# Kernel tuning notes

Hardware: AMD Instinct MI355X
Metric: run time of the kernel (lower is better)

The kernel has to match this reference:

```python
import jax, jax.numpy as jnp
import numpy as np

B, N, F, H, OUT = 64, 512, 128, 256, 6


def setup_inputs() -> dict:
    key = jax.random.key(0)
    ks = jax.random.split(key, 20)
    s = 0.02
    inp = {
        "x": jax.random.normal(ks[0], (B * N, F), dtype=jnp.float32),
        "edge_index": jax.random.randint(ks[1], (2, 16), 0, B * N),
        "edge_weight": jax.random.uniform(ks[2], (16,), dtype=jnp.float32),
        "batch": jnp.repeat(jnp.arange(B, dtype=jnp.int64), N),
        "sigma": jax.random.uniform(ks[3], (1,), dtype=jnp.float32),
        "Wg": s * jax.random.normal(ks[4], (F, F)), "bg": jnp.zeros((F,)),
        "Wrel0": s * jax.random.normal(ks[5], (F, H)), "Wroot0": s * jax.random.normal(ks[6], (F, H)), "brel0": jnp.zeros((H,)),
        "Wrel1": s * jax.random.normal(ks[7], (H, H)), "Wroot1": s * jax.random.normal(ks[8], (H, H)), "brel1": jnp.zeros((H,)),
        "Wrel2": s * jax.random.normal(ks[9], (H, H)), "Wroot2": s * jax.random.normal(ks[10], (H, H)), "brel2": jnp.zeros((H,)),
        "W1": s * jax.random.normal(ks[11], (H, H)), "b1": jnp.zeros((H,)),
        "Wout": s * jax.random.normal(ks[12], (H, OUT)), "bout": jnp.zeros((OUT,)),
    }
    return inp


def _forward(x, sigma, Wg, bg, Wrel0, Wroot0, brel0, Wrel1, Wroot1, brel1,
             Wrel2, Wroot2, brel2, W1, b1, Wout, bout):
    # gdmLinear
    h = x @ Wg + bg                      # [B*N, F]
    hw = h.reshape(B, N, -1)             # to_dense_batch (equal-size windows)
    # pairwise squared distances per window -> Gaussian kernel
    sq = jnp.sum(hw * hw, axis=-1)       # [B, N]
    dist = jnp.maximum(sq[:, :, None] + sq[:, None, :]
                       - 2.0 * jnp.einsum('bnf,bmf->bnm', hw, hw), 0.0)
    A = jnp.exp(-dist / (2.0 * sigma[0] ** 2))   # [B, N, N], all > 0
    A = A * (1.0 - jnp.eye(N, dtype=A.dtype))    # nonzero extraction drops self-loops

    def conv(h, Wrel, Wroot, brel):
        # GraphConv: out_i = W_rel @ sum_j A[j,i] * h_j + b_rel + W_root @ h_i
        agg = jnp.einsum('bji,bjf->bif', A, h)
        return agg @ Wrel + brel + h @ Wroot

    h = hw
    h = jax.nn.relu(conv(h, Wrel0, Wroot0, brel0))
    h = jax.nn.relu(conv(h, Wrel1, Wroot1, brel1))
    h = conv(h, Wrel2, Wroot2, brel2)
    g = jnp.mean(h, axis=1)              # global_mean_pool (equal-size graphs)
    g = jax.nn.relu(g @ W1 + b1)
    return g @ Wout + bout               # [B, OUT]


def reference(x, edge_index, edge_weight, batch, sigma, Wg, bg,
              Wrel0, Wroot0, brel0, Wrel1, Wroot1, brel1,
              Wrel2, Wroot2, brel2, W1, b1, Wout, bout):
    # edge_index / edge_weight / batch inputs are recomputed internally by GdmGNN
    return _forward(x, sigma, Wg, bg, Wrel0, Wroot0, brel0, Wrel1, Wroot1, brel1,
                    Wrel2, Wroot2, brel2, W1, b1, Wout, bout)
```

## Files before the change

### kernel.cpp

```cpp
#include <hip/hip_runtime.h>
#include <math.h>

#define Bsz 64
#define Nn 512
#define Ff 128
#define Hh 256
#define OUTD 6
#define MTOT (Bsz * Nn)

typedef __bf16 bf16x8 __attribute__((ext_vector_type(8)));
typedef float f32x4 __attribute__((ext_vector_type(4)));
typedef int int4v __attribute__((ext_vector_type(4)));
typedef unsigned short ushort4v __attribute__((ext_vector_type(4)));

__device__ __forceinline__ unsigned short f2bf(float f) {
    unsigned u = __float_as_uint(f);
    u += 0x7FFFu + ((u >> 16) & 1u);
    return (unsigned short)(u >> 16);
}
__device__ __forceinline__ float bf2f(unsigned short s) {
    return __uint_as_float(((unsigned)s) << 16);
}

#define SWZ(r) (((r) ^ ((r) >> 2)) & 3)

__device__ __forceinline__ void async_ld16(const unsigned short* g, unsigned short* l) {
    __builtin_amdgcn_global_load_lds(
        (const __attribute__((address_space(1))) void*)g,
        (__attribute__((address_space(3))) void*)l,
        16, 0, 0);
}

#define LDH 40
#define TSZ (128 * 32)

__global__ __launch_bounds__(512) void gemm_ah(
    const unsigned short* __restrict__ HT, const unsigned short* __restrict__ Arows,
    unsigned short* __restrict__ agg,
    int F, long strideHT, long strideA, long strideC, int mTiles)
{
    int id = blockIdx.x;
    int bz = id & 63;
    int t = id >> 6;
    int bx = t % mTiles;
    int by = t / mTiles;

    HT += (long)bz * strideHT;
    Arows += (long)bz * strideA;
    agg += (long)bz * strideC;

    __shared__ unsigned short As[2 * TSZ];
    __shared__ unsigned short Bs[2 * TSZ];

    int tid = threadIdx.x;
    int lane = tid & 63;
    int wave = tid >> 6;
    int quad = lane >> 4, l16 = lane & 15;
    int wm = (wave >> 1) * 32, wn = (wave & 1) * 64;
    int m0 = bx * 128, n0 = by * 128;

    int sr = lane >> 2, sc = lane & 3;

    f32x4 acc[2][4] = {};

    auto issue = [&](int g) {
        int kk = g << 5;
        unsigned short* Ad = As + (g & 1) * TSZ;
        unsigned short* Bd = Bs + (g & 1) * TSZ;
        int r = wave * 16 + sr;
        int c = sc ^ SWZ(r);
        async_ld16(HT + (long)(m0 + r) * Nn + kk + c * 8, Ad + (wave * 16) * 32);
        async_ld16(Arows + (long)(n0 + r) * Nn + kk + c * 8, Bd + (wave * 16) * 32);
    };

    issue(0);
    for (int g = 0; g < (Nn >> 5); ++g) {
        __syncthreads();
        if (g + 1 < (Nn >> 5)) issue(g + 1);
        const unsigned short* Ab = As + (g & 1) * TSZ;
        const unsigned short* Bb = Bs + (g & 1) * TSZ;
        bf16x8 af[2], bfr[4];
        #pragma unroll
        for (int i = 0; i < 2; ++i) {
            int r = wm + i * 16 + l16;
            af[i] = *(const bf16x8*)&Ab[r * 32 + (quad ^ SWZ(r)) * 8];
        }
        #pragma unroll
        for (int j = 0; j < 4; ++j) {
            int r = wn + j * 16 + l16;
            bfr[j] = *(const bf16x8*)&Bb[r * 32 + (quad ^ SWZ(r)) * 8];
        }
        #pragma unroll
        for (int i = 0; i < 2; ++i)
            #pragma unroll
            for (int j = 0; j < 4; ++j)
                acc[i][j] = __builtin_amdgcn_mfma_f32_16x16x32_bf16(
                    af[i], bfr[j], acc[i][j], 0, 0, 0);
    }

    #pragma unroll
    for (int i = 0; i < 2; ++i) {
        int f = m0 + wm + i * 16 + quad * 4;
        #pragma unroll
        for (int j = 0; j < 4; ++j) {
            int node = n0 + wn + j * 16 + l16;
            f32x4 v = acc[i][j];
            ushort4v p;
            p[0] = f2bf(v[0]); p[1] = f2bf(v[1]); p[2] = f2bf(v[2]); p[3] = f2bf(v[3]);
            *(ushort4v*)&agg[(long)node * F + f] = p;
        }
    }
}

__global__ __launch_bounds__(512) void dense_t(
    const unsigned short* __restrict__ A0, const unsigned short* __restrict__ B0T,
    const unsigned short* __restrict__ A1, const unsigned short* __restrict__ B1T,
    const float* __restrict__ bias,
    unsigned short* __restrict__ outB, unsigned short* __restrict__ outT,
    int K0, int K1, int relu)
{
    int m0 = blockIdx.x * 128;
    int n0 = blockIdx.y * 128;

    __shared__ unsigned short As[2 * TSZ];
    __shared__ unsigned short Bs[2 * TSZ];

    int tid = threadIdx.x;
    int lane = tid & 63;
    int wave = tid >> 6;
    int quad = lane >> 4, l16 = lane & 15;
    int wm = (wave >> 1) * 32, wn = (wave & 1) * 64;

    int sr = lane >> 2, sc = lane & 3;

    int T0 = K0 >> 5, T1 = K1 >> 5;
    int T = T0 + T1;

    f32x4 acc[2][4] = {};

    auto issue = [&](int g) {
        const unsigned short* Ag; const unsigned short* Bg; int Kg, kk;
        if (g < T0) { Ag = A0; Bg = B0T; Kg = K0; kk = g << 5; }
        else        { Ag = A1; Bg = B1T; Kg = K1; kk = (g - T0) << 5; }
        unsigned short* Ad = As + (g & 1) * TSZ;
        unsigned short* Bd = Bs + (g & 1) * TSZ;
        int r = wave * 16 + sr;
        int c = sc ^ SWZ(r);
        async_ld16(Ag + (long)(m0 + r) * Kg + kk + c * 8, Ad + (wave * 16) * 32);
        async_ld16(Bg + (long)(n0 + r) * Kg + kk + c * 8, Bd + (wave * 16) * 32);
    };

    issue(0);
    for (int g = 0; g < T; ++g) {
        __syncthreads();
        if (g + 1 < T) issue(g + 1);
        const unsigned short* Ab = As + (g & 1) * TSZ;
        const unsigned short* Bb = Bs + (g & 1) * TSZ;
        bf16x8 af[2], bfr[4];
        #pragma unroll
        for (int i = 0; i < 2; ++i) {
            int r = wm + i * 16 + l16;
            af[i] = *(const bf16x8*)&Ab[r * 32 + (quad ^ SWZ(r)) * 8];
        }
        #pragma unroll
        for (int j = 0; j < 4; ++j) {
            int r = wn + j * 16 + l16;
            bfr[j] = *(const bf16x8*)&Bb[r * 32 + (quad ^ SWZ(r)) * 8];
        }
        #pragma unroll
        for (int i = 0; i < 2; ++i)
            #pragma unroll
            for (int j = 0; j < 4; ++j)
                acc[i][j] = __builtin_amdgcn_mfma_f32_16x16x32_bf16(
                    af[i], bfr[j], acc[i][j], 0, 0, 0);
    }

    #pragma unroll
    for (int i = 0; i < 2; ++i) {
        int of = m0 + wm + i * 16 + quad * 4;
        float b0 = bias[of + 0], b1 = bias[of + 1];
        float b2 = bias[of + 2], b3 = bias[of + 3];
        #pragma unroll
        for (int j = 0; j < 4; ++j) {
            int node = n0 + wn + j * 16 + l16;
            f32x4 v = acc[i][j];
            float o0 = v[0] + b0, o1 = v[1] + b1, o2 = v[2] + b2, o3 = v[3] + b3;
            if (relu) {
                o0 = fmaxf(o0, 0.f); o1 = fmaxf(o1, 0.f);
                o2 = fmaxf(o2, 0.f); o3 = fmaxf(o3, 0.f);
            }
            ushort4v p;
            p[0] = f2bf(o0); p[1] = f2bf(o1); p[2] = f2bf(o2); p[3] = f2bf(o3);
            *(ushort4v*)&outB[(long)node * Hh + of] = p;
            if (outT) {
                long base = ((long)(node >> 9) * Hh) * 512 + (node & 511);
                outT[base + (long)(of + 0) * 512] = p[0];
                outT[base + (long)(of + 1) * 512] = p[1];
                outT[base + (long)(of + 2) * 512] = p[2];
                outT[base + (long)(of + 3) * 512] = p[3];
            }
        }
    }
}

__global__ __launch_bounds__(256) void prep_h0(
    const float* __restrict__ x, const float* __restrict__ Wg,
    const float* __restrict__ bg,
    const float* __restrict__ Wrel0, const float* __restrict__ Wroot0,
    const float* __restrict__ Wrel1, const float* __restrict__ Wroot1,
    unsigned short* __restrict__ T0, unsigned short* __restrict__ T1,
    unsigned short* __restrict__ T2, unsigned short* __restrict__ T3,
    unsigned short* __restrict__ WgT,
    float* __restrict__ w,
    unsigned short* __restrict__ h0b, unsigned short* __restrict__ h0T,
    float* __restrict__ sqv)
{
    if (blockIdx.x < 960) {
        int idx = blockIdx.x * 256 + threadIdx.x;
        if (idx >= 212992) { w[idx - 212992] = 0.f; return; }
        if (idx >= 196608) {
            int e = idx - 196608;
            int o = e >> 7, i = e & 127;
            WgT[e] = f2bf(Wg[(long)i * 128 + o]);
            return;
        }
        const float* src; unsigned short* dst; int kin; int e;
        if      (idx <  32768) { src = Wrel0;  dst = T0; kin = 128; e = idx; }
        else if (idx <  65536) { src = Wroot0; dst = T1; kin = 128; e = idx - 32768; }
        else if (idx < 131072) { src = Wrel1;  dst = T2; kin = 256; e = idx - 65536; }
        else                   { src = Wroot1; dst = T3; kin = 256; e = idx - 131072; }
        int o = (kin == 128) ? (e >> 7) : (e >> 8);
        int i = e & (kin - 1);
        dst[e] = f2bf(src[(long)i * 256 + o]);
        return;
    }

    __shared__ unsigned short As[128 * LDH];
    __shared__ unsigned short Bs[128 * LDH];
    __shared__ float rsq[128];

    int tid = threadIdx.x;
    int lane = tid & 63;
    int wave = tid >> 6;
    int quad = lane >> 4, l16 = lane & 15;
    int wm = (wave >> 1) * 64, wn = (wave & 1) * 64;
    int m0 = (blockIdx.x - 960) * 128;

    f32x4 acc[4][4] = {};

    for (int k0 = 0; k0 < Ff; k0 += 32) {
        __syncthreads();
        #pragma unroll
        for (int l = 0; l < 2; ++l) {
            int idx = tid + l * 256;
            int r = idx >> 2, ch = idx & 3;
            const float* px = x + (long)(m0 + r) * Ff + k0 + ch * 8;
            float4 xa = *(const float4*)px;
            float4 xb = *(const float4*)(px + 4);
            ushort4v pa, pb;
            pa[0] = f2bf(xa.x); pa[1] = f2bf(xa.y); pa[2] = f2bf(xa.z); pa[3] = f2bf(xa.w);
            pb[0] = f2bf(xb.x); pb[1] = f2bf(xb.y); pb[2] = f2bf(xb.z); pb[3] = f2bf(xb.w);
            *(ushort4v*)&As[r * LDH + ch * 8] = pa;
            *(ushort4v*)&As[r * LDH + ch * 8 + 4] = pb;
            int kk = k0 + ch * 8;
            ushort4v qa, qb;
            #pragma unroll
            for (int u = 0; u < 4; ++u) qa[u] = f2bf(Wg[(long)(kk + u) * 128 + r]);
            #pragma unroll
            for (int u = 0; u < 4; ++u) qb[u] = f2bf(Wg[(long)(kk + 4 + u) * 128 + r]);
            *(ushort4v*)&Bs[r * LDH + ch * 8] = qa;
            *(ushort4v*)&Bs[r * LDH + ch * 8 + 4] = qb;
        }
        __syncthreads();
        bf16x8 af[4], bfr[4];
        #pragma unroll
        for (int i = 0; i < 4; ++i)
            af[i] = *(const bf16x8*)&As[(wm + i * 16 + l16) * LDH + quad * 8];
        #pragma unroll
        for (int j = 0; j < 4; ++j)
            bfr[j] = *(const bf16x8*)&Bs[(wn + j * 16 + l16) * LDH + quad * 8];
        #pragma unroll
        for (int i = 0; i < 4; ++i)
            #pragma unroll
            for (int j = 0; j < 4; ++j)
                acc[i][j] = __builtin_amdgcn_mfma_f32_16x16x32_bf16(
                    af[i], bfr[j], acc[i][j], 0, 0, 0);
    }

    if (tid < 128) rsq[tid] = 0.f;
    __syncthreads();

    #pragma unroll
    for (int i = 0; i < 4; ++i) {
        int lrow = wm + i * 16 + quad * 4;
        int mb = m0 + lrow;
        float rp0 = 0.f, rp1 = 0.f, rp2 = 0.f, rp3 = 0.f;
        #pragma unroll
        for (int j = 0; j < 4; ++j) {
            int n = wn + j * 16 + l16;
            f32x4 v = acc[i][j];
            float bv = bg[n];
            unsigned short s0 = f2bf(v[0] + bv), s1 = f2bf(v[1] + bv);
            unsigned short s2 = f2bf(v[2] + bv), s3 = f2bf(v[3] + bv);
            h0b[(long)(mb + 0) * Ff + n] = s0;
            h0b[(long)(mb + 1) * Ff + n] = s1;
            h0b[(long)(mb + 2) * Ff + n] = s2;
            h0b[(long)(mb + 3) * Ff + n] = s3;
            ushort4v p; p[0] = s0; p[1] = s1; p[2] = s2; p[3] = s3;
            long ti = ((long)(mb >> 9) * Ff + n) * 512 + (mb & 511);
            *(ushort4v*)&h0T[ti] = p;
            float f0 = bf2f(s0), f1 = bf2f(s1), f2 = bf2f(s2), f3 = bf2f(s3);
            rp0 += f0 * f0; rp1 += f1 * f1; rp2 += f2 * f2; rp3 += f3 * f3;
        }
        #pragma unroll
        for (int m = 1; m < 16; m <<= 1) {
            rp0 += __shfl_xor(rp0, m);
            rp1 += __shfl_xor(rp1, m);
            rp2 += __shfl_xor(rp2, m);
            rp3 += __shfl_xor(rp3, m);
        }
        if (l16 == 0) {
            atomicAdd(&rsq[lrow + 0], rp0);
            atomicAdd(&rsq[lrow + 1], rp1);
            atomicAdd(&rsq[lrow + 2], rp2);
            atomicAdd(&rsq[lrow + 3], rp3);
        }
    }
    __syncthreads();
    if (tid < 128) sqv[m0 + tid] = rsq[tid];
}

__global__ __launch_bounds__(512) void gram_A_mfma(
    const unsigned short* __restrict__ h0b, const float* __restrict__ sqv,
    const float* __restrict__ sigma, unsigned short* __restrict__ Aout,
    float* __restrict__ w)
{
    const int ti_[10] = {0,0,0,0,1,1,1,2,2,3};
    const int tj_[10] = {0,1,2,3,1,2,3,2,3,3};
    int id = blockIdx.x;
    int b = id & 63;
    int tt = id >> 6;
    int i0 = ti_[tt] * 128, j0 = tj_[tt] * 128;
    bool offdiag = (i0 != j0);

    const unsigned short* H = h0b + (long)b * Nn * Ff;
    const float* SQ = sqv + (long)b * Nn;
    unsigned short* Ab = Aout + (long)b * Nn * Nn;

    __shared__ unsigned short Is[2 * TSZ];
    __shared__ unsigned short Js[2 * TSZ];
    __shared__ float rsum[128];
    __shared__ float csum[128];

    int tid = threadIdx.x;
    int lane = tid & 63;
    int wave = tid >> 6;
    int quad = lane >> 4, l16 = lane & 15;
    int wm = (wave >> 1) * 32, wn = (wave & 1) * 64;

    int sr = lane >> 2, sc = lane & 3;

    f32x4 acc[2][4] = {};

    auto issue = [&](int g) {
        int kk = g << 5;
        unsigned short* Id = Is + (g & 1) * TSZ;
        unsigned short* Jd = Js + (g & 1) * TSZ;
        int r = wave * 16 + sr;
        int c = sc ^ SWZ(r);
        async_ld16(H + (long)(i0 + r) * Ff + kk + c * 8, Id + (wave * 16) * 32);
        async_ld16(H + (long)(j0 + r) * Ff + kk + c * 8, Jd + (wave * 16) * 32);
    };

    issue(0);
    for (int g = 0; g < (Ff >> 5); ++g) {
        __syncthreads();
        if (g + 1 < (Ff >> 5)) issue(g + 1);
        const unsigned short* Ib = Is + (g & 1) * TSZ;
        const unsigned short* Jb = Js + (g & 1) * TSZ;
        bf16x8 af[2], bfr[4];
        #pragma unroll
        for (int i = 0; i < 2; ++i) {
            int r = wm + i * 16 + l16;
            af[i] = *(const bf16x8*)&Ib[r * 32 + (quad ^ SWZ(r)) * 8];
        }
        #pragma unroll
        for (int j = 0; j < 4; ++j) {
            int r = wn + j * 16 + l16;
            bfr[j] = *(const bf16x8*)&Jb[r * 32 + (quad ^ SWZ(r)) * 8];
        }
        #pragma unroll
        for (int i = 0; i < 2; ++i)
            #pragma unroll
            for (int j = 0; j < 4; ++j)
                acc[i][j] = __builtin_amdgcn_mfma_f32_16x16x32_bf16(
                    af[i], bfr[j], acc[i][j], 0, 0, 0);
    }

    if (tid < 128) { rsum[tid] = 0.f; csum[tid] = 0.f; }
    __syncthreads();

    float s = sigma[0];
    float inv2s2 = 1.0f / (2.0f * s * s);
    float cj[4] = {0.f, 0.f, 0.f, 0.f};
    #pragma unroll
    for (int i = 0; i < 2; ++i) {
        int lrow = wm + i * 16 + quad * 4;
        int rb = i0 + lrow;
        float rs0 = 0.f, rs1 = 0.f, rs2 = 0.f, rs3 = 0.f;
        #pragma unroll
        for (int j = 0; j < 4; ++j) {
            int c = j0 + wn + j * 16 + l16;
            float sqc = SQ[c];
            f32x4 v = acc[i][j];
            ushort4v pk;
            float av[4];
            #pragma unroll
            for (int r4 = 0; r4 < 4; ++r4) {
                int r = rb + r4;
                float d = fmaxf(SQ[r] + sqc - 2.0f * v[r4], 0.0f);
                unsigned short a = (r == c) ? (unsigned short)0
                                            : f2bf(__expf(-d * inv2s2));
                pk[r4] = a;
                av[r4] = bf2f(a);
            }
            *(ushort4v*)&Ab[(long)c * Nn + rb] = pk;
            if (offdiag) {
                Ab[(long)(rb + 0) * Nn + c] = pk[0];
                Ab[(long)(rb + 1) * Nn + c] = pk[1];
                Ab[(long)(rb + 2) * Nn + c] = pk[2];
                Ab[(long)(rb + 3) * Nn + c] = pk[3];
                cj[j] += av[0] + av[1] + av[2] + av[3];
            }
            rs0 += av[0]; rs1 += av[1]; rs2 += av[2]; rs3 += av[3];
        }
        #pragma unroll
        for (int m = 1; m < 16; m <<= 1) {
            rs0 += __shfl_xor(rs0, m);
            rs1 += __shfl_xor(rs1, m);
            rs2 += __shfl_xor(rs2, m);
            rs3 += __shfl_xor(rs3, m);
        }
        if (l16 == 0) {
            atomicAdd(&rsum[lrow + 0], rs0);
            atomicAdd(&rsum[lrow + 1], rs1);
            atomicAdd(&rsum[lrow + 2], rs2);
            atomicAdd(&rsum[lrow + 3], rs3);
        }
    }
    if (offdiag) {
        #pragma unroll
        for (int j = 0; j < 4; ++j) {
            cj[j] += __shfl_xor(cj[j], 16);
            cj[j] += __shfl_xor(cj[j], 32);
        }
        if (quad == 0) {
            #pragma unroll
            for (int j = 0; j < 4; ++j)
                atomicAdd(&csum[wn + j * 16 + l16], cj[j]);
        }
    }
    __syncthreads();
    if (tid < 128) {
        atomicAdd(&w[(long)b * Nn + i0 + tid], rsum[tid]);
        if (offdiag) atomicAdd(&w[(long)b * Nn + j0 + tid], csum[tid]);
    }
}

__global__ __launch_bounds__(256) void reduce_h2(
    const unsigned short* __restrict__ h2b, const float* __restrict__ w,
    float* __restrict__ vpart, float* __restrict__ mpart)
{
    int b = blockIdx.x;
    int jc = blockIdx.y;
    int c = threadIdx.x;
    const unsigned short* H = h2b + ((long)b * Nn + jc * 64) * Hh + c;
    const float* wp = w + (long)b * Nn + jc * 64;
    float vp = 0.f, mp = 0.f;
    #pragma unroll 4
    for (int j = 0; j < 64; ++j) {
        float val = bf2f(H[(long)j * Hh]);
        mp += val;
        vp += wp[j] * val;
    }
    long o = ((long)b * 8 + jc) * Hh + c;
    vpart[o] = vp;
    mpart[o] = mp;
}

__global__ __launch_bounds__(256) void head_kernel(
    const float* __restrict__ vpart, const float* __restrict__ mpart,
    const float* __restrict__ Wrel2, const float* __restrict__ Wroot2,
    const float* __restrict__ brel2,
    const float* __restrict__ W1, const float* __restrict__ b1,
    const float* __restrict__ Wout, const float* __restrict__ bout,
    float* __restrict__ out)
{
    int b = blockIdx.x;
    int j = threadIdx.x;
    __shared__ float vs[Hh], ms[Hh], gs[Hh], g2[Hh];
    float vp = 0.f, mp = 0.f;
    #pragma unroll
    for (int p = 0; p < 8; ++p) {
        long o = ((long)b * 8 + p) * Hh + j;
        vp += vpart[o];
        mp += mpart[o];
    }
    vs[j] = vp * (1.0f / (float)Nn);
    ms[j] = mp * (1.0f / (float)Nn);
    __syncthreads();
    float s = brel2[j];
    for (int c = 0; c < Hh; ++c)
        s += vs[c] * Wrel2[c * Hh + j] + ms[c] * Wroot2[c * Hh + j];
    gs[j] = s;
    __syncthreads();
    float t = b1[j];
    for (int k = 0; k < Hh; ++k) t += gs[k] * W1[k * Hh + j];
    g2[j] = fmaxf(t, 0.f);
    __syncthreads();
    if (j < OUTD) {
        float s2 = bout[j];
        for (int k = 0; k < Hh; ++k) s2 += g2[k] * Wout[k * OUTD + j];
        out[b * OUTD + j] = s2;
    }
}

extern "C" void kernel_launch(void* const* d_in, const int* in_sizes, int n_in,
                              void* d_out, int out_size, void* d_ws, size_t ws_size,
                              hipStream_t stream) {
    const float* x      = (const float*)d_in[0];
    const float* sigma  = (const float*)d_in[4];
    const float* Wg     = (const float*)d_in[5];
    const float* bg     = (const float*)d_in[6];
    const float* Wrel0  = (const float*)d_in[7];
    const float* Wroot0 = (const float*)d_in[8];
    const float* brel0  = (const float*)d_in[9];
    const float* Wrel1  = (const float*)d_in[10];
    const float* Wroot1 = (const float*)d_in[11];
    const float* brel1  = (const float*)d_in[12];
    const float* Wrel2  = (const float*)d_in[13];
    const float* Wroot2 = (const float*)d_in[14];
    const float* brel2  = (const float*)d_in[15];
    const float* W1     = (const float*)d_in[16];
    const float* b1     = (const float*)d_in[17];
    const float* Wout   = (const float*)d_in[18];
    const float* bout   = (const float*)d_in[19];
    float* out = (float*)d_out;

    char* ws = (char*)d_ws;
    unsigned short* WgT  = (unsigned short*)(ws + 0);
    unsigned short* h0b  = (unsigned short*)(ws + 16777216);
    unsigned short* h0T  = (unsigned short*)(ws + 25165824);
    float*          sq   = (float*)(ws + 33554432);
    unsigned short* Aadj = (unsigned short*)(ws + 33685504);
    unsigned short* agg  = (unsigned short*)(ws + 67239936);
    unsigned short* h1b  = (unsigned short*)(ws + 84017152);
    unsigned short* h1T  = (unsigned short*)(ws + 100794368);
    unsigned short* h2b  = (unsigned short*)(ws + 117571584);
    unsigned short* WrelT0  = (unsigned short*)(ws + 167903232);
    unsigned short* WrootT0 = (unsigned short*)(ws + 167968768);
    unsigned short* WrelT1  = (unsigned short*)(ws + 168034304);
    unsigned short* WrootT1 = (unsigned short*)(ws + 168165376);
    float*          w     = (float*)(ws + 168558592);
    float*          vpart = (float*)(ws + 168689664);
    float*          mpart = (float*)(ws + 169213952);

    prep_h0<<<1216, 256, 0, stream>>>(x, Wg, bg, Wrel0, Wroot0, Wrel1, Wroot1,
                                      WrelT0, WrootT0, WrelT1, WrootT1, WgT,
                                      w, h0b, h0T, sq);

    gram_A_mfma<<<dim3(10 * Bsz, 1, 1), 512, 0, stream>>>(h0b, sq, sigma, Aadj, w);

    gemm_ah<<<dim3(4 * Bsz, 1, 1), 512, 0, stream>>>(
        h0T, Aadj, agg, Ff,
        (long)Ff * Nn, (long)Nn * Nn, (long)Nn * Ff, 1);
    dense_t<<<dim3(2, MTOT / 128), 512, 0, stream>>>(
        WrelT0, agg, WrootT0, h0b, brel0, h1b, h1T, Ff, Ff, 1);

    gemm_ah<<<dim3(8 * Bsz, 1, 1), 512, 0, stream>>>(
        h1T, Aadj, agg, Hh,
        (long)Hh * Nn, (long)Nn * Nn, (long)Nn * Hh, 2);
    dense_t<<<dim3(2, MTOT / 128), 512, 0, stream>>>(
        WrelT1, agg, WrootT1, h1b, brel1, h2b, nullptr, Hh, Hh, 1);

    reduce_h2<<<dim3(Bsz, 8), 256, 0, stream>>>(h2b, w, vpart, mpart);
    head_kernel<<<Bsz, 256, 0, stream>>>(vpart, mpart, Wrel2, Wroot2, brel2,
                                         W1, b1, Wout, bout, out);
}
```

Baseline: 235.8 us.

## Fuse final pooling into dense_t and compute full Gram tiles without symmetric mirroring

The weighted and plain per-graph column sums of h2 are now computed in the epilogue of the second dense_t via a template flag, so h2 is no longer written to memory and the separate reduce_h2 kernel is dropped. The Gram/adjacency kernel changes from 10 upper-triangular tiles with scattered transposed mirror writes to all 16 tiles per graph, each doing only coalesced writes and row sums. This trades about 60% more Gram MFMA and exp work for removing strided scalar stores, column-sum atomics and one kernel launch plus an h2 round trip.

Result: faster. 229.6 us (-2.6%).

```diff
diff --git a/kernel.cpp b/kernel.cpp
--- a/kernel.cpp
+++ b/kernel.cpp
@@ -112,11 +112,13 @@
     }
 }
 
+template<int POOL>
 __global__ __launch_bounds__(512) void dense_t(
     const unsigned short* __restrict__ A0, const unsigned short* __restrict__ B0T,
     const unsigned short* __restrict__ A1, const unsigned short* __restrict__ B1T,
     const float* __restrict__ bias,
     unsigned short* __restrict__ outB, unsigned short* __restrict__ outT,
+    const float* __restrict__ w, float* __restrict__ vpart, float* __restrict__ mpart,
     int K0, int K1, int relu)
 {
     int m0 = blockIdx.x * 128;
@@ -124,6 +126,8 @@
 
     __shared__ unsigned short As[2 * TSZ];
     __shared__ unsigned short Bs[2 * TSZ];
+    __shared__ float vred[128];
+    __shared__ float mred[128];
 
     int tid = threadIdx.x;
     int lane = tid & 63;
@@ -175,11 +179,19 @@
                     af[i], bfr[j], acc[i][j], 0, 0, 0);
     }
 
+    if (POOL) {
+        if (tid < 128) { vred[tid] = 0.f; mred[tid] = 0.f; }
+        __syncthreads();
+    }
+
     #pragma unroll
     for (int i = 0; i < 2; ++i) {
-        int of = m0 + wm + i * 16 + quad * 4;
+        int lf = wm + i * 16 + quad * 4;
+        int of = m0 + lf;
         float b0 = bias[of + 0], b1 = bias[of + 1];
         float b2 = bias[of + 2], b3 = bias[of + 3];
+        float vp0 = 0.f, vp1 = 0.f, vp2 = 0.f, vp3 = 0.f;
+        float mp0 = 0.f, mp1 = 0.f, mp2 = 0.f, mp3 = 0.f;
         #pragma unroll
         for (int j = 0; j < 4; ++j) {
             int node = n0 + wn + j * 16 + l16;
@@ -191,14 +203,45 @@
             }
             ushort4v p;
             p[0] = f2bf(o0); p[1] = f2bf(o1); p[2] = f2bf(o2); p[3] = f2bf(o3);
-            *(ushort4v*)&outB[(long)node * Hh + of] = p;
-            if (outT) {
-                long base = ((long)(node >> 9) * Hh) * 512 + (node & 511);
-                outT[base + (long)(of + 0) * 512] = p[0];
-                outT[base + (long)(of + 1) * 512] = p[1];
-                outT[base + (long)(of + 2) * 512] = p[2];
-                outT[base + (long)(of + 3) * 512] = p[3];
+            if (!POOL) {
+                *(ushort4v*)&outB[(long)node * Hh + of] = p;
+                if (outT) {
+                    long base = ((long)(node >> 9) * Hh) * 512 + (node & 511);
+                    outT[base + (long)(of + 0) * 512] = p[0];
+                    outT[base + (long)(of + 1) * 512] = p[1];
+                    outT[base + (long)(of + 2) * 512] = p[2];
+                    outT[base + (long)(of + 3) * 512] = p[3];
+                }
+            } else {
+                float wv = w[node];
+                float h0v = bf2f(p[0]), h1v = bf2f(p[1]);
+                float h2v = bf2f(p[2]), h3v = bf2f(p[3]);
+                vp0 += wv * h0v; vp1 += wv * h1v; vp2 += wv * h2v; vp3 += wv * h3v;
+                mp0 += h0v; mp1 += h1v; mp2 += h2v; mp3 += h3v;
             }
+        }
+        if (POOL) {
+            #pragma unroll
+            for (int m = 1; m < 16; m <<= 1) {
+                vp0 += __shfl_xor(vp0, m); vp1 += __shfl_xor(vp1, m);
+                vp2 += __shfl_xor(vp2, m); vp3 += __shfl_xor(vp3, m);
+                mp0 += __shfl_xor(mp0, m); mp1 += __shfl_xor(mp1, m);
+                mp2 += __shfl_xor(mp2, m); mp3 += __shfl_xor(mp3, m);
+            }
+            if (l16 == 0) {
+                atomicAdd(&vred[lf + 0], vp0); atomicAdd(&vred[lf + 1], vp1);
+                atomicAdd(&vred[lf + 2], vp2); atomicAdd(&vred[lf + 3], vp3);
+                atomicAdd(&mred[lf + 0], mp0); atomicAdd(&mred[lf + 1], mp1);
+                atomicAdd(&mred[lf + 2], mp2); atomicAdd(&mred[lf + 3], mp3);
+            }
+        }
+    }
+    if (POOL) {
+        __syncthreads();
+        if (tid < 128) {
+            long o = (long)blockIdx.y * Hh + m0 + tid;
+            vpart[o] = vred[tid];
+            mpart[o] = mred[tid];
         }
     }
 }
@@ -335,13 +378,10 @@
     const float* __restrict__ sigma, unsigned short* __restrict__ Aout,
     float* __restrict__ w)
 {
-    const int ti_[10] = {0,0,0,0,1,1,1,2,2,3};
-    const int tj_[10] = {0,1,2,3,1,2,3,2,3,3};
     int id = blockIdx.x;
     int b = id & 63;
-    int tt = id >> 6;
-    int i0 = ti_[tt] * 128, j0 = tj_[tt] * 128;
-    bool offdiag = (i0 != j0);
+    int t = id >> 6;
+    int i0 = (t & 3) * 128, j0 = (t >> 2) * 128;
 
     const unsigned short* H = h0b + (long)b * Nn * Ff;
     const float* SQ = sqv + (long)b * Nn;
@@ -350,7 +390,6 @@
     __shared__ unsigned short Is[2 * TSZ];
     __shared__ unsigned short Js[2 * TSZ];
     __shared__ float rsum[128];
-    __shared__ float csum[128];
 
     int tid = threadIdx.x;
     int lane = tid & 63;
@@ -397,12 +436,11 @@
                     af[i], bfr[j], acc[i][j], 0, 0, 0);
     }
 
-    if (tid < 128) { rsum[tid] = 0.f; csum[tid] = 0.f; }
+    if (tid < 128) rsum[tid] = 0.f;
     __syncthreads();
 
     float s = sigma[0];
     float inv2s2 = 1.0f / (2.0f * s * s);
-    float cj[4] = {0.f, 0.f, 0.f, 0.f};
     #pragma unroll
     for (int i = 0; i < 2; ++i) {
         int lrow = wm + i * 16 + quad * 4;
@@ -425,13 +463,6 @@
                 av[r4] = bf2f(a);
             }
             *(ushort4v*)&Ab[(long)c * Nn + rb] = pk;
-            if (offdiag) {
-                Ab[(long)(rb + 0) * Nn + c] = pk[0];
-                Ab[(long)(rb + 1) * Nn + c] = pk[1];
-                Ab[(long)(rb + 2) * Nn + c] = pk[2];
-                Ab[(long)(rb + 3) * Nn + c] = pk[3];
-                cj[j] += av[0] + av[1] + av[2] + av[3];
-            }
             rs0 += av[0]; rs1 += av[1]; rs2 += av[2]; rs3 += av[3];
         }
         #pragma unroll
@@ -448,44 +479,8 @@
             atomicAdd(&rsum[lrow + 3], rs3);
         }
     }
-    if (offdiag) {
-        #pragma unroll
-        for (int j = 0; j < 4; ++j) {
-            cj[j] += __shfl_xor(cj[j], 16);
-            cj[j] += __shfl_xor(cj[j], 32);
-        }
-        if (quad == 0) {
-            #pragma unroll
-            for (int j = 0; j < 4; ++j)
-                atomicAdd(&csum[wn + j * 16 + l16], cj[j]);
-        }
-    }
-    __syncthreads();
-    if (tid < 128) {
-        atomicAdd(&w[(long)b * Nn + i0 + tid], rsum[tid]);
-        if (offdiag) atomicAdd(&w[(long)b * Nn + j0 + tid], csum[tid]);
-    }
-}
-
-__global__ __launch_bounds__(256) void reduce_h2(
-    const unsigned short* __restrict__ h2b, const float* __restrict__ w,
-    float* __restrict__ vpart, float* __restrict__ mpart)
-{
-    int b = blockIdx.x;
-    int jc = blockIdx.y;
-    int c = threadIdx.x;
-    const unsigned short* H = h2b + ((long)b * Nn + jc * 64) * Hh + c;
-    const float* wp = w + (long)b * Nn + jc * 64;
-    float vp = 0.f, mp = 0.f;
-    #pragma unroll 4
-    for (int j = 0; j < 64; ++j) {
-        float val = bf2f(H[(long)j * Hh]);
-        mp += val;
-        vp += wp[j] * val;
-    }
-    long o = ((long)b * 8 + jc) * Hh + c;
-    vpart[o] = vp;
-    mpart[o] = mp;
+    __syncthreads();
+    if (tid < 128) atomicAdd(&w[(long)b * Nn + i0 + tid], rsum[tid]);
 }
 
 __global__ __launch_bounds__(256) void head_kernel(
@@ -501,8 +496,8 @@
     __shared__ float vs[Hh], ms[Hh], gs[Hh], g2[Hh];
     float vp = 0.f, mp = 0.f;
     #pragma unroll
-    for (int p = 0; p < 8; ++p) {
-        long o = ((long)b * 8 + p) * Hh + j;
+    for (int p = 0; p < 4; ++p) {
+        long o = ((long)(b * 4 + p)) * Hh + j;
         vp += vpart[o];
         mp += mpart[o];
     }
@@ -556,34 +551,34 @@
     unsigned short* agg  = (unsigned short*)(ws + 67239936);
     unsigned short* h1b  = (unsigned short*)(ws + 84017152);
     unsigned short* h1T  = (unsigned short*)(ws + 100794368);
-    unsigned short* h2b  = (unsigned short*)(ws + 117571584);
     unsigned short* WrelT0  = (unsigned short*)(ws + 167903232);
     unsigned short* WrootT0 = (unsigned short*)(ws + 167968768);
     unsigned short* WrelT1  = (unsigned short*)(ws + 168034304);
     unsigned short* WrootT1 = (unsigned short*)(ws + 168165376);
     float*          w     = (float*)(ws + 168558592);
     float*          vpart = (float*)(ws + 168689664);
-    float*          mpart = (float*)(ws + 169213952);
+    float*          mpart = (float*)(ws + 168951808);
 
     prep_h0<<<1216, 256, 0, stream>>>(x, Wg, bg, Wrel0, Wroot0, Wrel1, Wroot1,
                                       WrelT0, WrootT0, WrelT1, WrootT1, WgT,
                                       w, h0b, h0T, sq);
 
-    gram_A_mfma<<<dim3(10 * Bsz, 1, 1), 512, 0, stream>>>(h0b, sq, sigma, Aadj, w);
+    gram_A_mfma<<<dim3(16 * Bsz, 1, 1), 512, 0, stream>>>(h0b, sq, sigma, Aadj, w);
 
     gemm_ah<<<dim3(4 * Bsz, 1, 1), 512, 0, stream>>>(
         h0T, Aadj, agg, Ff,
         (long)Ff * Nn, (long)Nn * Nn, (long)Nn * Ff, 1);
-    dense_t<<<dim3(2, MTOT / 128), 512, 0, stream>>>(
-        WrelT0, agg, WrootT0, h0b, brel0, h1b, h1T, Ff, Ff, 1);
+    dense_t<0><<<dim3(2, MTOT / 128), 512, 0, stream>>>(
+        WrelT0, agg, WrootT0, h0b, brel0, h1b, h1T,
+        nullptr, nullptr, nullptr, Ff, Ff, 1);
 
     gemm_ah<<<dim3(8 * Bsz, 1, 1), 512, 0, stream>>>(
         h1T, Aadj, agg, Hh,
         (long)Hh * Nn, (long)Nn * Nn, (long)Nn * Hh, 2);
-    dense_t<<<dim3(2, MTOT / 128), 512, 0, stream>>>(
-        WrelT1, agg, WrootT1, h1b, brel1, h2b, nullptr, Hh, Hh, 1);
-
-    reduce_h2<<<dim3(Bsz, 8), 256, 0, stream>>>(h2b, w, vpart, mpart);
+    dense_t<1><<<dim3(2, MTOT / 128), 512, 0, stream>>>(
+        WrelT1, agg, WrootT1, h1b, brel1, nullptr, nullptr,
+        w, vpart, mpart, Hh, Hh, 1);
+
     head_kernel<<<Bsz, 256, 0, stream>>>(vpart, mpart, Wrel2, Wroot2, brel2,
                                          W1, b1, Wout, bout, out);
 }
```
